# Kernel tuning notes

Measured on AMD Instinct MI355X. Metric: run time of the kernel, lower is better.

The kernel has to match this reference:

```python
import jax, jax.numpy as jnp
import numpy as np

N_HEAD = 8
SPAN = 32
BN_EPS = 1e-5


def setup_inputs() -> dict:
    key = jax.random.key(0)
    k1, k2, k3 = jax.random.split(key, 3)
    d_model = 256
    hc = d_model // N_HEAD
    x = jax.random.normal(k1, (4, d_model, 32, 32, 32), dtype=jnp.float32)
    qkv_weight = jax.random.normal(k2, (2 * d_model, d_model), dtype=jnp.float32) * np.sqrt(1.0 / d_model)
    relative = jax.random.normal(k3, (2 * hc, 2 * SPAN - 1), dtype=jnp.float32) * np.sqrt(1.0 / hc)
    gamma = jnp.ones((2 * d_model,), dtype=jnp.float32)
    beta = jnp.zeros((2 * d_model,), dtype=jnp.float32)
    return {"x": x, "qkv_weight": qkv_weight, "relative": relative, "gamma": gamma, "beta": beta}


def _batchnorm1d_train(x, gamma, beta):
    # x: (N, C, L); training-mode BN with batch statistics (biased var)
    mean = x.mean(axis=(0, 2), keepdims=True)
    var = x.var(axis=(0, 2), keepdims=True)
    return (x - mean) * jax.lax.rsqrt(var + BN_EPS) * gamma[None, :, None] + beta[None, :, None]


def reference(x, qkv_weight, relative, gamma, beta):
    B, C, H, W, T = x.shape
    hc = C // N_HEAD
    # width=False: permute (B,C,H,W,T) -> (B,T,W,C,H); attention along H
    xp = jnp.transpose(x, (0, 4, 3, 1, 2)).reshape(B * T * W, C, H)
    # 1x1 conv == channel matmul: (2C,C) x (N,C,H) -> (N,2C,H)
    qkv = jnp.einsum('oc,ncl->nol', qkv_weight, xp)
    qkv = qkv.reshape(B * T * W, N_HEAD, 2 * hc, H)
    q = qkv[:, :, : hc // 2]          # (N, nh, hc/2, H)
    k = qkv[:, :, hc // 2: hc]        # (N, nh, hc/2, H)
    v = qkv[:, :, hc:]                # (N, nh, hc,   H)
    # relative position table gather: all_emb[c,i,j] = relative[c, i+j]
    idx = jnp.arange(SPAN)[:, None] + jnp.arange(SPAN)[None, :]
    all_emb = relative[:, idx]        # (2hc, span, span)
    q_emb = all_emb[: hc // 2]
    k_emb = all_emb[hc // 2: hc]
    v_emb = all_emb[hc:]
    qr = jnp.einsum('nhci,cij->nhij', q, q_emb)
    kr = jnp.einsum('nhci,cij->nhij', k, k_emb)
    qk = jnp.einsum('nhci,nhcj->nhij', q, k)
    sim = jax.nn.softmax(qk + qr + kr, axis=-1)      # (N, nh, H, H)
    sv = jnp.einsum('nhij,nhcj->nhci', sim, v)       # (N, nh, hc, H)
    sve = jnp.einsum('nhij,cij->nhci', sim, v_emb)   # (N, nh, hc, H)
    # cat along last dim then view (N, 2C, H) == interleave sv/sve per (h,c)
    stacked = jnp.stack([sv, sve], axis=3).reshape(B * T * W, 2 * C, H)
    out = _batchnorm1d_train(stacked, gamma, beta)
    out = out.reshape(B, T, W, C, 2, H).sum(axis=4)  # (B,T,W,C,H)
    return jnp.transpose(out, (0, 3, 4, 2, 1))       # (B,C,H,W,T)
```

## Files before the change

### kernel.cpp

```cpp
#include <hip/hip_runtime.h>
#include <hip/hip_bf16.h>


typedef __attribute__((ext_vector_type(8))) short short8;
typedef __attribute__((ext_vector_type(16))) float f32x16;

__device__ inline unsigned short f2bu(float f) {
  __hip_bfloat16 h = __float2bfloat16(f);
  return *(unsigned short*)&h;
}

#define MFMA32(A, B, C) __builtin_amdgcn_mfma_f32_32x32x16_bf16(A, B, C, 0, 0, 0)

constexpr int S_I = 646;
constexpr int S_C = 10;

__global__ __launch_bounds__(256) void k0_wsplit(
    const float* __restrict__ W, unsigned short* __restrict__ Whi,
    unsigned short* __restrict__ Wlo) {
  const int i = blockIdx.x * 256 + threadIdx.x;
  const float w = W[i];
  const unsigned u = __float_as_uint(w);
  const float fhi = __uint_as_float(u & 0xFFFF0000u);
  const float lo = w - fhi;
  Whi[i] = (unsigned short)(u >> 16);
  Wlo[i] = (unsigned short)(__float_as_uint(lo) >> 16);
}

__device__ inline void gload16(const float* g, float* l) {
  __builtin_amdgcn_global_load_lds(
      (const __attribute__((address_space(1))) unsigned int*)(g),
      (__attribute__((address_space(3))) unsigned int*)(l), 16, 0, 0);
}

__global__ __launch_bounds__(256) void k1_mfma(
    const unsigned short* __restrict__ Whi, const unsigned short* __restrict__ Wlo,
    const float* __restrict__ x, __hip_bfloat16* __restrict__ qkv) {
  __shared__ float Bs[32 * 128];

  const int td = threadIdx.x, bx = blockIdx.x;
  const int otile = bx & 3, nt = (bx >> 2) & 255, b = bx >> 10;
  const int w = nt & 31, i0 = (nt >> 5) << 2;
  const int o0 = otile * 128;
  const float* xb = x + (size_t)b * 256 * 32768;

  const int wid = td >> 6, l = td & 63, h = l >> 5, n = l & 31;
  const int wo = wid >> 1, wn = wid & 1;

  const f32x16 zf = {0, 0, 0, 0, 0, 0, 0, 0, 0, 0, 0, 0, 0, 0, 0, 0};
  f32x16 acc[2][2];
#pragma unroll
  for (int it = 0; it < 2; ++it)
#pragma unroll
    for (int jt = 0; jt < 2; ++jt) acc[it][jt] = zf;

  for (int k0 = 0; k0 < 256; k0 += 32) {
    __syncthreads();
#pragma unroll
    for (int r = 0; r < 4; ++r) {
      const int idx = r * 256 + td;
      const int kk = idx >> 5, u = idx & 31;
      const int di = (u >> 1) & 3, tcq = u >> 3, toff = (u & 1) * 4;
      gload16(xb + (size_t)(k0 + kk) * 32768 + (i0 + di) * 1024 + w * 32 +
                  tcq * 8 + toff,
              Bs + idx * 4);
    }
    __syncthreads();

#pragma unroll
    for (int kf = 0; kf < 2; ++kf) {
      const int kbase = k0 + kf * 16 + h * 8;
      short8 ahi[2], alo[2];
#pragma unroll
      for (int it = 0; it < 2; ++it) {
        const int row = o0 + wo * 64 + it * 32 + n;
        ahi[it] = *(const short8*)(Whi + (size_t)row * 256 + kbase);
        alo[it] = *(const short8*)(Wlo + (size_t)row * 256 + kbase);
      }
      short8 bhi[2], blo[2];
#pragma unroll
      for (int jt = 0; jt < 2; ++jt) {
        const int col = wn * 64 + jt * 32 + n;
#pragma unroll
        for (int e = 0; e < 8; ++e) {
          const float f = Bs[(kf * 16 + h * 8 + e) * 128 + col];
          const unsigned u = __float_as_uint(f);
          bhi[jt][e] = (short)(u >> 16);
          const float fl = f - __uint_as_float(u & 0xFFFF0000u);
          blo[jt][e] = (short)(__float_as_uint(fl) >> 16);
        }
      }
#pragma unroll
      for (int it = 0; it < 2; ++it)
#pragma unroll
        for (int jt = 0; jt < 2; ++jt) {
          acc[it][jt] = MFMA32(ahi[it], bhi[jt], acc[it][jt]);
          acc[it][jt] = MFMA32(ahi[it], blo[jt], acc[it][jt]);
          acc[it][jt] = MFMA32(alo[it], bhi[jt], acc[it][jt]);
        }
    }
  }

  __hip_bfloat16* qb2 = qkv + ((size_t)((b * 32 + w) * 8 + otile * 2 + wo)) * 65536 +
                        (size_t)(wn * 2) * 16384 + i0 * 8;
#pragma unroll
  for (int jt = 0; jt < 2; ++jt) {
    __hip_bfloat16* bjt = qb2 + jt * 16384;
#pragma unroll
    for (int it = 0; it < 2; ++it) {
#pragma unroll
      for (int r = 0; r < 16; ++r) {
        const int ch = it * 32 + (r & 3) + 8 * (r >> 2) + 4 * h;
        bjt[ch * 256 + n] = __float2bfloat16(acc[it][jt][r]);
      }
    }
  }
}

__global__ __launch_bounds__(256, 3) void k2_attn_mfma(
    const __hip_bfloat16* __restrict__ qkv, const float* __restrict__ rel,
    unsigned int* __restrict__ stk2, float* __restrict__ stats) {
  __shared__ __align__(16) __hip_bfloat16 slab[20672];
  __shared__ __align__(16) unsigned short Sbuf[4 * 1280];
  __shared__ float statb[4][32][4];

  const int bx = blockIdx.x;
  const int w = bx & 31, head = (bx >> 5) & 7, b = bx >> 8;
  const int td = threadIdx.x;
  const int wid = td >> 6, l = td & 63, h = l >> 5, n = l & 31;

  short8 eqf[2], ekf[2], evf[4];
#pragma unroll
  for (int dt = 0; dt < 2; ++dt)
#pragma unroll
    for (int e = 0; e < 8; ++e) {
      int c = h * 8 + e, d = dt * 32 + n;
      eqf[dt][e] = (d < 63) ? (short)f2bu(rel[c * 63 + d]) : (short)0;
      ekf[dt][e] = (d < 63) ? (short)f2bu(rel[(16 + c) * 63 + d]) : (short)0;
    }
#pragma unroll
  for (int kh = 0; kh < 4; ++kh)
#pragma unroll
    for (int e = 0; e < 8; ++e) {
      int d = kh * 16 + h * 8 + e;
      evf[kh][e] = (d < 63) ? (short)f2bu(rel[(32 + n) * 63 + d]) : (short)0;
    }
  short8 ones;
#pragma unroll
  for (int e = 0; e < 8; ++e) ones[e] = (short)0x3F80;

  const __hip_bfloat16* qbase = qkv + ((size_t)((b * 32 + w) * 8 + head)) * 65536;
  unsigned int* sb = stk2 + ((size_t)((b * 8 + head) * 32 + w)) * 32768;
  unsigned short* Sb = Sbuf + wid * 1280;

  const f32x16 zf = {0, 0, 0, 0, 0, 0, 0, 0, 0, 0, 0, 0, 0, 0, 0, 0};
  float st0 = 0, st1 = 0, st2 = 0, st3 = 0;

  for (int tc = 0; tc < 4; ++tc) {
    const int t0 = tc * 8;
    __syncthreads();
    for (int r = 0; r < 8; ++r) {
      int idx = td + 256 * r;
      const uint4 dat = *(const uint4*)(qbase + (size_t)tc * 16384 + (size_t)idx * 8);
      unsigned int* lp = (unsigned int*)(slab + (idx & 31) * S_I + (idx >> 5) * S_C);
      lp[0] = dat.x; lp[1] = dat.y; lp[2] = dat.z; lp[3] = dat.w;
    }
    __syncthreads();
    for (int u = 0; u < 2; ++u) {
      const int tt = 2 * wid + u;
      const int t = t0 + tt;
      short8 aq, ak;
#pragma unroll
      for (int e = 0; e < 8; ++e) {
        aq[e] = *(const short*)&slab[n * S_I + (h * 8 + e) * S_C + tt];
        ak[e] = *(const short*)&slab[n * S_I + (16 + h * 8 + e) * S_C + tt];
      }
      f32x16 qkD = MFMA32(aq, ak, zf);
      f32x16 Rq0 = MFMA32(aq, eqf[0], zf);
      f32x16 Rq1 = MFMA32(aq, eqf[1], zf);
      f32x16 Rk0 = MFMA32(ak, ekf[0], zf);
      f32x16 Rk1 = MFMA32(ak, ekf[1], zf);
#pragma unroll
      for (int r = 0; r < 16; ++r) {
        int rowr = (r & 3) + 8 * (r >> 2) + 4 * h;
        int d = rowr + n;
        int src = (d & 31) + 32 * h;
        float vq0 = __shfl(Rq0[r], src);
        float vq1 = __shfl(Rq1[r], src);
        float vk0 = __shfl(Rk0[r], src);
        float vk1 = __shfl(Rk1[r], src);
        float s = qkD[r] + (d < 32 ? vq0 + vk0 : vq1 + vk1);
        Sb[rowr * 40 + n] = f2bu(__expf(s));
      }
      short8 bv0, bv1;
#pragma unroll
      for (int e = 0; e < 8; ++e) {
        int j0 = h * 8 + e, j1 = 16 + h * 8 + e;
        bv0[e] = *(const short*)&slab[j0 * S_I + (32 + n) * S_C + tt];
        bv1[e] = *(const short*)&slab[j1 * S_I + (32 + n) * S_C + tt];
      }
      short8 as0 = *(const short8*)(Sb + n * 40 + h * 8);
      short8 as1 = *(const short8*)(Sb + n * 40 + 16 + h * 8);
      f32x16 svD = MFMA32(as1, bv1, MFMA32(as0, bv0, zf));
      f32x16 sumD = MFMA32(as1, ones, MFMA32(as0, ones, zf));
      f32x16 sveD = zf;
#pragma unroll
      for (int kh = 0; kh < 4; ++kh) {
        short8 ap;
#pragma unroll
        for (int e = 0; e < 8; ++e) {
          int k = kh * 16 + h * 8 + e;
          int jj = k - n;
          unsigned short raw = Sb[n * 40 + (jj & 31)];
          ap[e] = ((unsigned)jj < 32u) ? (short)raw : (short)0;
        }
        sveD = MFMA32(ap, evf[kh], sveD);
      }
#pragma unroll
      for (int r = 0; r < 16; ++r) {
        int rowr = (r & 3) + 8 * (r >> 2) + 4 * h;
        float inv = 1.0f / sumD[r];
        float svn = svD[r] * inv, sven = sveD[r] * inv;
        st0 += svn; st1 += svn * svn; st2 += sven; st3 += sven * sven;
        unsigned int pk = (unsigned int)f2bu(svn) | ((unsigned int)f2bu(sven) << 16);
        sb[((size_t)rowr * 32 + t) * 32 + n] = pk;
      }
    }
  }
  st0 += __shfl_xor(st0, 32); st1 += __shfl_xor(st1, 32);
  st2 += __shfl_xor(st2, 32); st3 += __shfl_xor(st3, 32);
  if (h == 0) {
    statb[wid][n][0] = st0; statb[wid][n][1] = st1;
    statb[wid][n][2] = st2; statb[wid][n][3] = st3;
  }
  __syncthreads();
  if (td < 32) {
    float a0 = 0, a1 = 0, a2 = 0, a3 = 0;
    for (int wv = 0; wv < 4; ++wv) {
      a0 += statb[wv][td][0]; a1 += statb[wv][td][1];
      a2 += statb[wv][td][2]; a3 += statb[wv][td][3];
    }
    const int o2 = head * 64 + 2 * td;
    atomicAdd(&stats[o2], a0);
    atomicAdd(&stats[o2 + 1], a2);
    atomicAdd(&stats[512 + o2], a1);
    atomicAdd(&stats[512 + o2 + 1], a3);
  }
}

__global__ __launch_bounds__(256) void k3_finalize2(
    const unsigned int* __restrict__ stk2, const float* __restrict__ stats,
    const float* __restrict__ gamma, const float* __restrict__ beta,
    float* __restrict__ out) {
  __shared__ float trans[32][33];
  __shared__ float s_sc[64], s_sh[64];
  const int bx = blockIdx.x;
  const int w = bx & 31, head = (bx >> 5) & 7, b = bx >> 8;
  const int td = threadIdx.x;
  if (td < 64) {
    const int o2 = head * 64 + td;
    const float NINV = 1.f / 131072.f;
    float m = stats[o2] * NINV;
    float v = stats[512 + o2] * NINV - m * m;
    float sc = gamma[o2] * rsqrtf(v + 1e-5f);
    s_sc[td] = sc;
    s_sh[td] = beta[o2] - m * sc;
  }
  __syncthreads();
  const unsigned int* pb = stk2 + ((size_t)((b * 8 + head) * 32 + w)) * 32768;
  float* ob = out + ((size_t)(b * 256 + head * 32)) * 32768 + w * 32;
  const int t = td >> 3, c0 = (td & 7) * 4;
  for (int i = 0; i < 32; ++i) {
    const uint4 dat = *(const uint4*)(pb + (size_t)i * 1024 + td * 4);
    unsigned int dws[4] = {dat.x, dat.y, dat.z, dat.w};
#pragma unroll
    for (int q = 0; q < 4; ++q) {
      int c = c0 + q;
      float sv = __uint_as_float((dws[q] & 0xFFFFu) << 16);
      float sve = __uint_as_float(dws[q] & 0xFFFF0000u);
      trans[c][t] = sv * s_sc[2 * c] + sve * s_sc[2 * c + 1] + s_sh[2 * c] + s_sh[2 * c + 1];
    }
    __syncthreads();
    {
      const int t2 = td & 31;
#pragma unroll
      for (int cc = 0; cc < 4; ++cc) {
        int c = (td >> 5) + 8 * cc;
        ob[(size_t)c * 32768 + (size_t)i * 1024 + t2] = trans[c][t2];
      }
    }
    __syncthreads();
  }
}

extern "C" void kernel_launch(void* const* d_in, const int* in_sizes, int n_in,
                              void* d_out, int out_size, void* d_ws, size_t ws_size,
                              hipStream_t stream) {
  const float* x        = (const float*)d_in[0];
  const float* qkv_w    = (const float*)d_in[1];
  const float* relative = (const float*)d_in[2];
  const float* gamma    = (const float*)d_in[3];
  const float* beta     = (const float*)d_in[4];
  float* out = (float*)d_out;

  __hip_bfloat16* qkv = (__hip_bfloat16*)d_ws;
  unsigned int* stk2 = (unsigned int*)((char*)d_ws + (size_t)134217728);
  float* stats = (float*)((char*)d_ws + (size_t)268435456);
  unsigned short* Whi = (unsigned short*)stk2;
  unsigned short* Wlo = Whi + 131072;

  hipMemsetAsync(stats, 0, 1024 * sizeof(float), stream);
  k0_wsplit<<<dim3(512), dim3(256), 0, stream>>>(qkv_w, Whi, Wlo);
  k1_mfma<<<dim3(4096), dim3(256), 0, stream>>>(Whi, Wlo, x, qkv);
  k2_attn_mfma<<<dim3(1024), dim3(256), 0, stream>>>(qkv, relative, stk2, stats);
  k3_finalize2<<<dim3(1024), dim3(256), 0, stream>>>(stk2, stats, gamma, beta, out);
}
```

Measured before the change: 627.4 us.

## Load x directly into registers in QKV GEMM and batch finalize transposes by four

The QKV projection kernel no longer stages x tiles through LDS with global_load_lds and barriers. Each lane now loads its eight strided k-values straight from global memory into registers and splits them into bf16 hi/lo there, with the k loop partially unrolled. The finalize kernel processes four H-rows per LDS transpose round, which cuts barriers per row and keeps more loads in flight. The trade-off is many uncoalesced scalar global loads with a 32768-element stride and no reuse of x across waves that share columns, which may raise memory traffic.

```diff
diff --git a/kernel.cpp b/kernel.cpp
--- a/kernel.cpp
+++ b/kernel.cpp
@@ -27,17 +27,9 @@
   Wlo[i] = (unsigned short)(__float_as_uint(lo) >> 16);
 }
 
-__device__ inline void gload16(const float* g, float* l) {
-  __builtin_amdgcn_global_load_lds(
-      (const __attribute__((address_space(1))) unsigned int*)(g),
-      (__attribute__((address_space(3))) unsigned int*)(l), 16, 0, 0);
-}
-
 __global__ __launch_bounds__(256) void k1_mfma(
     const unsigned short* __restrict__ Whi, const unsigned short* __restrict__ Wlo,
     const float* __restrict__ x, __hip_bfloat16* __restrict__ qkv) {
-  __shared__ float Bs[32 * 128];
-
   const int td = threadIdx.x, bx = blockIdx.x;
   const int otile = bx & 3, nt = (bx >> 2) & 255, b = bx >> 10;
   const int w = nt & 31, i0 = (nt >> 5) << 2;
@@ -47,6 +39,12 @@
   const int wid = td >> 6, l = td & 63, h = l >> 5, n = l & 31;
   const int wo = wid >> 1, wn = wid & 1;
 
+  const int colsp0 = (i0 + (n >> 3)) * 1024 + w * 32 + (wn * 2) * 8 + (n & 7);
+  const float* px0 = xb + colsp0 + (size_t)(h * 8) * 32768;
+  const float* px1 = px0 + 8;
+  const unsigned short* pwh = Whi + (size_t)(o0 + wo * 64 + n) * 256 + h * 8;
+  const unsigned short* pwl = Wlo + (size_t)(o0 + wo * 64 + n) * 256 + h * 8;
+
   const f32x16 zf = {0, 0, 0, 0, 0, 0, 0, 0, 0, 0, 0, 0, 0, 0, 0, 0};
   f32x16 acc[2][2];
 #pragma unroll
@@ -54,50 +52,40 @@
 #pragma unroll
     for (int jt = 0; jt < 2; ++jt) acc[it][jt] = zf;
 
-  for (int k0 = 0; k0 < 256; k0 += 32) {
-    __syncthreads();
-#pragma unroll
-    for (int r = 0; r < 4; ++r) {
-      const int idx = r * 256 + td;
-      const int kk = idx >> 5, u = idx & 31;
-      const int di = (u >> 1) & 3, tcq = u >> 3, toff = (u & 1) * 4;
-      gload16(xb + (size_t)(k0 + kk) * 32768 + (i0 + di) * 1024 + w * 32 +
-                  tcq * 8 + toff,
-              Bs + idx * 4);
-    }
-    __syncthreads();
-
-#pragma unroll
-    for (int kf = 0; kf < 2; ++kf) {
-      const int kbase = k0 + kf * 16 + h * 8;
-      short8 ahi[2], alo[2];
-#pragma unroll
-      for (int it = 0; it < 2; ++it) {
-        const int row = o0 + wo * 64 + it * 32 + n;
-        ahi[it] = *(const short8*)(Whi + (size_t)row * 256 + kbase);
-        alo[it] = *(const short8*)(Wlo + (size_t)row * 256 + kbase);
-      }
-      short8 bhi[2], blo[2];
-#pragma unroll
-      for (int jt = 0; jt < 2; ++jt) {
-        const int col = wn * 64 + jt * 32 + n;
-#pragma unroll
-        for (int e = 0; e < 8; ++e) {
-          const float f = Bs[(kf * 16 + h * 8 + e) * 128 + col];
-          const unsigned u = __float_as_uint(f);
-          bhi[jt][e] = (short)(u >> 16);
-          const float fl = f - __uint_as_float(u & 0xFFFF0000u);
-          blo[jt][e] = (short)(__float_as_uint(fl) >> 16);
-        }
-      }
-#pragma unroll
-      for (int it = 0; it < 2; ++it)
-#pragma unroll
-        for (int jt = 0; jt < 2; ++jt) {
-          acc[it][jt] = MFMA32(ahi[it], bhi[jt], acc[it][jt]);
-          acc[it][jt] = MFMA32(ahi[it], blo[jt], acc[it][jt]);
-          acc[it][jt] = MFMA32(alo[it], bhi[jt], acc[it][jt]);
-        }
+#pragma unroll 4
+  for (int kf = 0; kf < 16; ++kf) {
+    const float* pk0 = px0 + (size_t)kf * 16 * 32768;
+    const float* pk1 = px1 + (size_t)kf * 16 * 32768;
+    float xv0[8], xv1[8];
+#pragma unroll
+    for (int e = 0; e < 8; ++e) {
+      xv0[e] = pk0[(size_t)e * 32768];
+      xv1[e] = pk1[(size_t)e * 32768];
+    }
+    short8 ahi[2], alo[2];
+#pragma unroll
+    for (int it = 0; it < 2; ++it) {
+      ahi[it] = *(const short8*)(pwh + it * (32 * 256) + kf * 16);
+      alo[it] = *(const short8*)(pwl + it * (32 * 256) + kf * 16);
+    }
+    short8 bhi0, blo0, bhi1, blo1;
+#pragma unroll
+    for (int e = 0; e < 8; ++e) {
+      const unsigned u0 = __float_as_uint(xv0[e]);
+      bhi0[e] = (short)(u0 >> 16);
+      blo0[e] = (short)(__float_as_uint(xv0[e] - __uint_as_float(u0 & 0xFFFF0000u)) >> 16);
+      const unsigned u1 = __float_as_uint(xv1[e]);
+      bhi1[e] = (short)(u1 >> 16);
+      blo1[e] = (short)(__float_as_uint(xv1[e] - __uint_as_float(u1 & 0xFFFF0000u)) >> 16);
+    }
+#pragma unroll
+    for (int it = 0; it < 2; ++it) {
+      acc[it][0] = MFMA32(ahi[it], bhi0, acc[it][0]);
+      acc[it][0] = MFMA32(ahi[it], blo0, acc[it][0]);
+      acc[it][0] = MFMA32(alo[it], bhi0, acc[it][0]);
+      acc[it][1] = MFMA32(ahi[it], bhi1, acc[it][1]);
+      acc[it][1] = MFMA32(ahi[it], blo1, acc[it][1]);
+      acc[it][1] = MFMA32(alo[it], bhi1, acc[it][1]);
     }
   }
 
@@ -252,7 +240,7 @@
     const unsigned int* __restrict__ stk2, const float* __restrict__ stats,
     const float* __restrict__ gamma, const float* __restrict__ beta,
     float* __restrict__ out) {
-  __shared__ float trans[32][33];
+  __shared__ float trans[4][32][33];
   __shared__ float s_sc[64], s_sh[64];
   const int bx = blockIdx.x;
   const int w = bx & 31, head = (bx >> 5) & 7, b = bx >> 8;
@@ -270,23 +258,28 @@
   const unsigned int* pb = stk2 + ((size_t)((b * 8 + head) * 32 + w)) * 32768;
   float* ob = out + ((size_t)(b * 256 + head * 32)) * 32768 + w * 32;
   const int t = td >> 3, c0 = (td & 7) * 4;
-  for (int i = 0; i < 32; ++i) {
-    const uint4 dat = *(const uint4*)(pb + (size_t)i * 1024 + td * 4);
-    unsigned int dws[4] = {dat.x, dat.y, dat.z, dat.w};
-#pragma unroll
-    for (int q = 0; q < 4; ++q) {
-      int c = c0 + q;
-      float sv = __uint_as_float((dws[q] & 0xFFFFu) << 16);
-      float sve = __uint_as_float(dws[q] & 0xFFFF0000u);
-      trans[c][t] = sv * s_sc[2 * c] + sve * s_sc[2 * c + 1] + s_sh[2 * c] + s_sh[2 * c + 1];
+  const int t2 = td & 31, cbase = td >> 5;
+  for (int i4 = 0; i4 < 32; i4 += 4) {
+#pragma unroll
+    for (int m = 0; m < 4; ++m) {
+      const uint4 dat = *(const uint4*)(pb + (size_t)(i4 + m) * 1024 + td * 4);
+      unsigned int dws[4] = {dat.x, dat.y, dat.z, dat.w};
+#pragma unroll
+      for (int q = 0; q < 4; ++q) {
+        int c = c0 + q;
+        float sv = __uint_as_float((dws[q] & 0xFFFFu) << 16);
+        float sve = __uint_as_float(dws[q] & 0xFFFF0000u);
+        trans[m][c][t] =
+            sv * s_sc[2 * c] + sve * s_sc[2 * c + 1] + s_sh[2 * c] + s_sh[2 * c + 1];
+      }
     }
     __syncthreads();
-    {
-      const int t2 = td & 31;
+#pragma unroll
+    for (int m = 0; m < 4; ++m) {
 #pragma unroll
       for (int cc = 0; cc < 4; ++cc) {
-        int c = (td >> 5) + 8 * cc;
-        ob[(size_t)c * 32768 + (size_t)i * 1024 + t2] = trans[c][t2];
+        int c = cbase + 8 * cc;
+        ob[(size_t)c * 32768 + (size_t)(i4 + m) * 1024 + t2] = trans[m][c][t2];
       }
     }
     __syncthreads();
```

Result: slower. 693.2 us (+10.5%).

## Double-buffer k1 LDS staging, reorder block mapping, batch finalize transpose by four rows

Applied to the files above, without the earlier changes.

k1 now uses two LDS buffers and issues the async global-to-LDS load for the next K slice before computing the current one, with one barrier per step instead of two. Its block index mapping is changed so the four output tiles sharing an x slice land in different block ranges. In the finalize kernel, four rows are loaded and transposed per barrier pair instead of one, which cuts synchronisation and gives more loads in flight. The costs are doubled LDS in k1 and a larger transpose buffer in finalize, which may reduce occupancy, and the new k1 ordering may lower L2 reuse of x across output tiles.

```diff
diff --git a/kernel.cpp b/kernel.cpp
--- a/kernel.cpp
+++ b/kernel.cpp
@@ -36,10 +36,10 @@
 __global__ __launch_bounds__(256) void k1_mfma(
     const unsigned short* __restrict__ Whi, const unsigned short* __restrict__ Wlo,
     const float* __restrict__ x, __hip_bfloat16* __restrict__ qkv) {
-  __shared__ float Bs[32 * 128];
+  __shared__ float Bs[2][32 * 128];
 
   const int td = threadIdx.x, bx = blockIdx.x;
-  const int otile = bx & 3, nt = (bx >> 2) & 255, b = bx >> 10;
+  const int nt = bx & 255, otile = (bx >> 8) & 3, b = bx >> 10;
   const int w = nt & 31, i0 = (nt >> 5) << 2;
   const int o0 = otile * 128;
   const float* xb = x + (size_t)b * 256 * 32768;
@@ -47,6 +47,7 @@
   const int wid = td >> 6, l = td & 63, h = l >> 5, n = l & 31;
   const int wo = wid >> 1, wn = wid & 1;
 
+  const int sidx = td;
   const f32x16 zf = {0, 0, 0, 0, 0, 0, 0, 0, 0, 0, 0, 0, 0, 0, 0, 0};
   f32x16 acc[2][2];
 #pragma unroll
@@ -54,22 +55,28 @@
 #pragma unroll
     for (int jt = 0; jt < 2; ++jt) acc[it][jt] = zf;
 
-  for (int k0 = 0; k0 < 256; k0 += 32) {
-    __syncthreads();
-#pragma unroll
-    for (int r = 0; r < 4; ++r) {
-      const int idx = r * 256 + td;
-      const int kk = idx >> 5, u = idx & 31;
-      const int di = (u >> 1) & 3, tcq = u >> 3, toff = (u & 1) * 4;
-      gload16(xb + (size_t)(k0 + kk) * 32768 + (i0 + di) * 1024 + w * 32 +
-                  tcq * 8 + toff,
-              Bs + idx * 4);
-    }
-    __syncthreads();
-
+#define STAGE_K1(K0, BUF)                                                         \
+  {                                                                               \
+    _Pragma("unroll") for (int r = 0; r < 4; ++r) {                               \
+      const int idx = r * 256 + sidx;                                             \
+      const int kk = idx >> 5, u = idx & 31;                                      \
+      const int di = (u >> 1) & 3, tcq = u >> 3, toff = (u & 1) * 4;              \
+      gload16(xb + (size_t)((K0) + kk) * 32768 + (i0 + di) * 1024 + w * 32 +      \
+                  tcq * 8 + toff,                                                 \
+              &Bs[BUF][idx * 4]);                                                 \
+    }                                                                             \
+  }
+
+  STAGE_K1(0, 0);
+  __syncthreads();
+
+  for (int step = 0; step < 8; ++step) {
+    const int cur = step & 1;
+    if (step < 7) STAGE_K1((step + 1) * 32, cur ^ 1);
+    const float* Bc = Bs[cur];
 #pragma unroll
     for (int kf = 0; kf < 2; ++kf) {
-      const int kbase = k0 + kf * 16 + h * 8;
+      const int kbase = step * 32 + kf * 16 + h * 8;
       short8 ahi[2], alo[2];
 #pragma unroll
       for (int it = 0; it < 2; ++it) {
@@ -83,7 +90,7 @@
         const int col = wn * 64 + jt * 32 + n;
 #pragma unroll
         for (int e = 0; e < 8; ++e) {
-          const float f = Bs[(kf * 16 + h * 8 + e) * 128 + col];
+          const float f = Bc[(kf * 16 + h * 8 + e) * 128 + col];
           const unsigned u = __float_as_uint(f);
           bhi[jt][e] = (short)(u >> 16);
           const float fl = f - __uint_as_float(u & 0xFFFF0000u);
@@ -99,7 +106,9 @@
           acc[it][jt] = MFMA32(alo[it], bhi[jt], acc[it][jt]);
         }
     }
-  }
+    __syncthreads();
+  }
+#undef STAGE_K1
 
   __hip_bfloat16* qb2 = qkv + ((size_t)((b * 32 + w) * 8 + otile * 2 + wo)) * 65536 +
                         (size_t)(wn * 2) * 16384 + i0 * 8;
@@ -252,7 +261,7 @@
     const unsigned int* __restrict__ stk2, const float* __restrict__ stats,
     const float* __restrict__ gamma, const float* __restrict__ beta,
     float* __restrict__ out) {
-  __shared__ float trans[32][33];
+  __shared__ float trans[4][32][33];
   __shared__ float s_sc[64], s_sh[64];
   const int bx = blockIdx.x;
   const int w = bx & 31, head = (bx >> 5) & 7, b = bx >> 8;
@@ -270,23 +279,28 @@
   const unsigned int* pb = stk2 + ((size_t)((b * 8 + head) * 32 + w)) * 32768;
   float* ob = out + ((size_t)(b * 256 + head * 32)) * 32768 + w * 32;
   const int t = td >> 3, c0 = (td & 7) * 4;
-  for (int i = 0; i < 32; ++i) {
-    const uint4 dat = *(const uint4*)(pb + (size_t)i * 1024 + td * 4);
-    unsigned int dws[4] = {dat.x, dat.y, dat.z, dat.w};
-#pragma unroll
-    for (int q = 0; q < 4; ++q) {
-      int c = c0 + q;
-      float sv = __uint_as_float((dws[q] & 0xFFFFu) << 16);
-      float sve = __uint_as_float(dws[q] & 0xFFFF0000u);
-      trans[c][t] = sv * s_sc[2 * c] + sve * s_sc[2 * c + 1] + s_sh[2 * c] + s_sh[2 * c + 1];
-    }
-    __syncthreads();
-    {
-      const int t2 = td & 31;
+  const int t2 = td & 31, cbase = td >> 5;
+  for (int i4 = 0; i4 < 32; i4 += 4) {
+#pragma unroll
+    for (int m = 0; m < 4; ++m) {
+      const uint4 dat = *(const uint4*)(pb + (size_t)(i4 + m) * 1024 + td * 4);
+      unsigned int dws[4] = {dat.x, dat.y, dat.z, dat.w};
+#pragma unroll
+      for (int q = 0; q < 4; ++q) {
+        int c = c0 + q;
+        float sv = __uint_as_float((dws[q] & 0xFFFFu) << 16);
+        float sve = __uint_as_float(dws[q] & 0xFFFF0000u);
+        trans[m][c][t] =
+            sv * s_sc[2 * c] + sve * s_sc[2 * c + 1] + s_sh[2 * c] + s_sh[2 * c + 1];
+      }
+    }
+    __syncthreads();
+#pragma unroll
+    for (int m = 0; m < 4; ++m) {
 #pragma unroll
       for (int cc = 0; cc < 4; ++cc) {
-        int c = (td >> 5) + 8 * cc;
-        ob[(size_t)c * 32768 + (size_t)i * 1024 + t2] = trans[c][t2];
+        int c = cbase + 8 * cc;
+        ob[(size_t)c * 32768 + (size_t)(i4 + m) * 1024 + t2] = trans[m][c][t2];
       }
     }
     __syncthreads();
```

Result: no change. 625.4 us (-0.3%).
